# Kernel tuning notes

Hardware: AMD Instinct MI355X
Metric: run time of the kernel (lower is better)

Reference implementation:

```python
import jax, jax.numpy as jnp
import numpy as np
from functools import partial


def _normalise(v):
    return v / jnp.linalg.norm(v, axis=-1, keepdims=True)


def _orthogonalise(source, ref):
    # NOTE: faithful to original: divides by ||ref|| (not ||ref||^2)
    coef = jnp.einsum('bs,bs->b', source, ref) / jnp.linalg.norm(ref, axis=-1)
    return source - coef[:, None] * ref


def _skew(u):
    # (B,3) -> (B,3,3) cross-product matrix [u]_x, column j = u x e_j
    ux, uy, uz = u[:, 0], u[:, 1], u[:, 2]
    z = jnp.zeros_like(ux)
    return jnp.stack([
        jnp.stack([z, -uz, uy], axis=-1),
        jnp.stack([uz, z, -ux], axis=-1),
        jnp.stack([-uy, ux, z], axis=-1),
    ], axis=1)


def _rotate_frames(e0, e1, e2, angles, planar):
    u = e2 if planar else e1
    I = jnp.eye(3, dtype=u.dtype)[None]            # (1,3,3)
    cosA = jnp.cos(angles)[:, None, None]
    sinA = jnp.sin(angles)[:, None, None]
    outer = u[:, :, None] * u[:, None, :]          # (B,3,3)
    R = cosA * I + sinA * _skew(u) + (1.0 - cosA) * outer
    e0 = _normalise(jnp.einsum('bij,bj->bi', R, e0))
    if planar:
        e1 = _normalise(jnp.einsum('bij,bj->bi', R, e1))
    e1 = _normalise(_orthogonalise(e1, e0))
    e2 = _normalise(jnp.cross(e0, e1))
    return e0, e1, e2


def setup_inputs() -> dict:
    key = jax.random.key(0)
    B, N = 8192, 1024
    ks = jax.random.split(key, 6)
    x0 = jnp.zeros((B, 3), dtype=jnp.float32)
    e0 = _normalise(jax.random.uniform(ks[0], (B, 3), dtype=jnp.float32))
    e1 = _normalise(_orthogonalise(jax.random.uniform(ks[1], (B, 3), dtype=jnp.float32), e0))
    e2 = _normalise(jnp.cross(e0, e1))
    speeds = jax.random.uniform(ks[2], (B, N), dtype=jnp.float32)
    planar_angles = jax.random.normal(ks[3], (B, N), dtype=jnp.float32) * 0.3
    nonplanar_angles = jax.random.normal(ks[4], (B, N), dtype=jnp.float32) * 0.1
    return {'x0': x0, 'e0': e0, 'e1': e1, 'e2': e2,
            'speeds': speeds, 'planar_angles': planar_angles,
            'nonplanar_angles': nonplanar_angles, 'T': N, 'dt': 1}


def reference(x0, e0, e1, e2, speeds, planar_angles, nonplanar_angles, T, dt):
    n_steps = int(T / dt)
    B = x0.shape[0]
    ts = jnp.arange(n_steps, dtype=jnp.float32) * float(dt)

    def step(carry, inp):
        x, e0, e1, e2 = carry
        sp, pa, na = inp
        e0, e1, e2 = _rotate_frames(e0, e1, e2, pa, planar=True)
        e0, e1, e2 = _rotate_frames(e0, e1, e2, na, planar=False)
        x = x + sp[:, None] * e0
        return (x, e0, e1, e2), x

    xs = (speeds.T[:n_steps], planar_angles.T[:n_steps], nonplanar_angles.T[:n_steps])
    _, X = jax.lax.scan(step, (x0, e0, e1, e2), xs)
    X = jnp.transpose(X, (1, 0, 2))                 # (B, n_steps, 3)
    states = jnp.zeros((B, n_steps), dtype=jnp.float32)  # abstract state, left as zeros
    return ts, X, states, speeds, planar_angles, nonplanar_angles
```

## Files before the change

kernel.cpp:

```cpp
#include <hip/hip_runtime.h>

#define TPB   256
#define LSTEP 16


__global__ __launch_bounds__(TPB) void particle_scan_kernel(
    const float* __restrict__ x0p,
    const float* __restrict__ e0p,
    const float* __restrict__ e1p,
    const float* __restrict__ e2p,
    const float* __restrict__ sp,
    const float* __restrict__ pa,
    const float* __restrict__ na,
    const int*   __restrict__ dtp,
    float* __restrict__ out,
    int B, int N)
{
    const int tid  = threadIdx.x;
    const int lane = tid & 63;
    const int b    = (int)blockIdx.x * (TPB / 64) + (tid >> 6);
    const long long BN = (long long)B * N;
    const long long off_X      = N;
    const long long off_states = off_X + BN * 3;
    const long long off_speeds = off_states + BN;
    const long long off_pa     = off_speeds + BN;
    const long long off_na     = off_pa + BN;

    {
        int flat = (int)blockIdx.x * TPB + tid;
        if (flat < N) out[flat] = (float)flat * (float)dtp[0];
    }

    const long long base = (long long)b * N + (long long)lane * LSTEP;

    float spv[LSTEP], pav[LSTEP], nav[LSTEP];
    {
        const float4* s4 = reinterpret_cast<const float4*>(sp + base);
        const float4* p4 = reinterpret_cast<const float4*>(pa + base);
        const float4* q4 = reinterpret_cast<const float4*>(na + base);
        float4* os = reinterpret_cast<float4*>(out + off_speeds + base);
        float4* op = reinterpret_cast<float4*>(out + off_pa     + base);
        float4* oq = reinterpret_cast<float4*>(out + off_na     + base);
        float4* oz = reinterpret_cast<float4*>(out + off_states + base);
        const float4 z4 = make_float4(0.f, 0.f, 0.f, 0.f);
        #pragma unroll
        for (int i = 0; i < LSTEP / 4; ++i) {
            float4 a = s4[i], bb = p4[i], cc = q4[i];
            os[i] = a; op[i] = bb; oq[i] = cc; oz[i] = z4;
            spv[4*i+0] = a.x;  spv[4*i+1] = a.y;  spv[4*i+2] = a.z;  spv[4*i+3] = a.w;
            pav[4*i+0] = bb.x; pav[4*i+1] = bb.y; pav[4*i+2] = bb.z; pav[4*i+3] = bb.w;
            nav[4*i+0] = cc.x; nav[4*i+1] = cc.y; nav[4*i+2] = cc.z; nav[4*i+3] = cc.w;
        }
    }

    float a0x = 1.f, a0y = 0.f, a0z = 0.f;
    float a1x = 0.f, a1y = 1.f, a1z = 0.f;
    float a2x = 0.f, a2y = 0.f, a2z = 1.f;
    float dx = 0.f, dy = 0.f, dz = 0.f;
    #pragma unroll
    for (int t = 0; t < LSTEP; ++t) {
        float s1, c1, s2, c2;
        __sincosf(pav[t], &s1, &c1);
        __sincosf(nav[t], &s2, &c2);
        float t0x = c1*a0x + s1*a1x, t0y = c1*a0y + s1*a1y, t0z = c1*a0z + s1*a1z;
        float t1x = c1*a1x - s1*a0x, t1y = c1*a1y - s1*a0y, t1z = c1*a1z - s1*a0z;
        float u0x = c2*t0x - s2*a2x, u0y = c2*t0y - s2*a2y, u0z = c2*t0z - s2*a2z;
        float u2x = c2*a2x + s2*t0x, u2y = c2*a2y + s2*t0y, u2z = c2*a2z + s2*t0z;
        a0x = u0x; a0y = u0y; a0z = u0z;
        a1x = t1x; a1y = t1y; a1z = t1z;
        a2x = u2x; a2y = u2y; a2z = u2z;
        float s = spv[t];
        dx = fmaf(s, a0x, dx); dy = fmaf(s, a0y, dy); dz = fmaf(s, a0z, dz);
    }

    #define SCAN_STEP(K)                                                          \
    {                                                                             \
        float o0x=__shfl_up(a0x,K), o0y=__shfl_up(a0y,K), o0z=__shfl_up(a0z,K);   \
        float o1x=__shfl_up(a1x,K), o1y=__shfl_up(a1y,K), o1z=__shfl_up(a1z,K);   \
        float o2x=__shfl_up(a2x,K), o2y=__shfl_up(a2y,K), o2z=__shfl_up(a2z,K);   \
        float odx=__shfl_up(dx,K),  ody=__shfl_up(dy,K),  odz=__shfl_up(dz,K);    \
        if (lane >= K) {                                                          \
            float n0x = a0x*o0x + a0y*o1x + a0z*o2x;                              \
            float n0y = a0x*o0y + a0y*o1y + a0z*o2y;                              \
            float n0z = a0x*o0z + a0y*o1z + a0z*o2z;                              \
            float n1x = a1x*o0x + a1y*o1x + a1z*o2x;                              \
            float n1y = a1x*o0y + a1y*o1y + a1z*o2y;                              \
            float n1z = a1x*o0z + a1y*o1z + a1z*o2z;                              \
            float n2x = a2x*o0x + a2y*o1x + a2z*o2x;                              \
            float n2y = a2x*o0y + a2y*o1y + a2z*o2y;                              \
            float n2z = a2x*o0z + a2y*o1z + a2z*o2z;                              \
            float ndx = odx + dx*o0x + dy*o1x + dz*o2x;                           \
            float ndy = ody + dx*o0y + dy*o1y + dz*o2y;                           \
            float ndz = odz + dx*o0z + dy*o1z + dz*o2z;                           \
            a0x=n0x; a0y=n0y; a0z=n0z;                                            \
            a1x=n1x; a1y=n1y; a1z=n1z;                                            \
            a2x=n2x; a2y=n2y; a2z=n2z;                                            \
            dx=ndx; dy=ndy; dz=ndz;                                               \
        }                                                                         \
    }
    SCAN_STEP(1) SCAN_STEP(2) SCAN_STEP(4) SCAN_STEP(8) SCAN_STEP(16) SCAN_STEP(32)
    #undef SCAN_STEP

    {
        float e0x=__shfl_up(a0x,1), e0y=__shfl_up(a0y,1), e0z=__shfl_up(a0z,1);
        float e1x=__shfl_up(a1x,1), e1y=__shfl_up(a1y,1), e1z=__shfl_up(a1z,1);
        float e2x=__shfl_up(a2x,1), e2y=__shfl_up(a2y,1), e2z=__shfl_up(a2z,1);
        float edx=__shfl_up(dx,1),  edy=__shfl_up(dy,1),  edz=__shfl_up(dz,1);
        if (lane == 0) {
            e0x=1.f; e0y=0.f; e0z=0.f;
            e1x=0.f; e1y=1.f; e1z=0.f;
            e2x=0.f; e2y=0.f; e2z=1.f;
            edx=0.f; edy=0.f; edz=0.f;
        }
        a0x=e0x; a0y=e0y; a0z=e0z;
        a1x=e1x; a1y=e1y; a1z=e1z;
        a2x=e2x; a2y=e2y; a2z=e2z;
        dx=edx; dy=edy; dz=edz;
    }

    float f0x = e0p[3*b], f0y = e0p[3*b+1], f0z = e0p[3*b+2];
    float f1x = e1p[3*b], f1y = e1p[3*b+1], f1z = e1p[3*b+2];
    float f2x = e2p[3*b], f2y = e2p[3*b+1], f2z = e2p[3*b+2];
    float Xx  = x0p[3*b], Xy  = x0p[3*b+1], Xz  = x0p[3*b+2];

    float g0x = a0x*f0x + a0y*f1x + a0z*f2x;
    float g0y = a0x*f0y + a0y*f1y + a0z*f2y;
    float g0z = a0x*f0z + a0y*f1z + a0z*f2z;
    float g1x = a1x*f0x + a1y*f1x + a1z*f2x;
    float g1y = a1x*f0y + a1y*f1y + a1z*f2y;
    float g1z = a1x*f0z + a1y*f1z + a1z*f2z;
    float g2x = a2x*f0x + a2y*f1x + a2z*f2x;
    float g2y = a2x*f0y + a2y*f1y + a2z*f2y;
    float g2z = a2x*f0z + a2y*f1z + a2z*f2z;
    Xx += dx*f0x + dy*f1x + dz*f2x;
    Xy += dx*f0y + dy*f1y + dz*f2y;
    Xz += dx*f0z + dy*f1z + dz*f2z;

    float* Xb = out + off_X + base * 3;
    #pragma unroll
    for (int t = 0; t < LSTEP; ++t) {
        float s1, c1, s2, c2;
        __sincosf(pav[t], &s1, &c1);
        __sincosf(nav[t], &s2, &c2);
        float t0x = c1*g0x + s1*g1x, t0y = c1*g0y + s1*g1y, t0z = c1*g0z + s1*g1z;
        float t1x = c1*g1x - s1*g0x, t1y = c1*g1y - s1*g0y, t1z = c1*g1z - s1*g0z;
        float u0x = c2*t0x - s2*g2x, u0y = c2*t0y - s2*g2y, u0z = c2*t0z - s2*g2z;
        float u2x = c2*g2x + s2*t0x, u2y = c2*g2y + s2*t0y, u2z = c2*g2z + s2*t0z;
        g0x = u0x; g0y = u0y; g0z = u0z;
        g1x = t1x; g1y = t1y; g1z = t1z;
        g2x = u2x; g2y = u2y; g2z = u2z;
        float s = spv[t];
        Xx = fmaf(s, g0x, Xx); Xy = fmaf(s, g0y, Xy); Xz = fmaf(s, g0z, Xz);
        Xb[3*t + 0] = Xx;
        Xb[3*t + 1] = Xy;
        Xb[3*t + 2] = Xz;
    }
}

extern "C" void kernel_launch(void* const* d_in, const int* in_sizes, int n_in,
                              void* d_out, int out_size, void* d_ws, size_t ws_size,
                              hipStream_t stream)
{
    const float* x0  = (const float*)d_in[0];
    const float* e0i = (const float*)d_in[1];
    const float* e1i = (const float*)d_in[2];
    const float* e2i = (const float*)d_in[3];
    const float* sp  = (const float*)d_in[4];
    const float* pa  = (const float*)d_in[5];
    const float* na  = (const float*)d_in[6];
    const int*   dtp = (const int*)d_in[8];

    int B = in_sizes[0] / 3;
    int N = in_sizes[4] / B;

    int nBlocks = B / (TPB / 64);
    particle_scan_kernel<<<dim3(nBlocks), dim3(TPB), 0, stream>>>(
        x0, e0i, e1i, e2i, sp, pa, na, dtp, (float*)d_out, B, N);
}
```

Baseline: 371.3 us.

## Store local displacement prefixes and replay via frame transform with float4 stores

Measured after the change: 404.1 us. 1.09x slower.

```diff
diff --git a/kernel.cpp b/kernel.cpp
--- a/kernel.cpp
+++ b/kernel.cpp
@@ -33,7 +33,12 @@
 
     const long long base = (long long)b * N + (long long)lane * LSTEP;
 
-    float spv[LSTEP], pav[LSTEP], nav[LSTEP];
+    float a0x = 1.f, a0y = 0.f, a0z = 0.f;
+    float a1x = 0.f, a1y = 1.f, a1z = 0.f;
+    float a2x = 0.f, a2y = 0.f, a2z = 1.f;
+    float dx = 0.f, dy = 0.f, dz = 0.f;
+    float dlx[LSTEP], dly[LSTEP], dlz[LSTEP];
+
     {
         const float4* s4 = reinterpret_cast<const float4*>(sp + base);
         const float4* p4 = reinterpret_cast<const float4*>(pa + base);
@@ -43,34 +48,33 @@
         float4* oq = reinterpret_cast<float4*>(out + off_na     + base);
         float4* oz = reinterpret_cast<float4*>(out + off_states + base);
         const float4 z4 = make_float4(0.f, 0.f, 0.f, 0.f);
+
         #pragma unroll
-        for (int i = 0; i < LSTEP / 4; ++i) {
-            float4 a = s4[i], bb = p4[i], cc = q4[i];
-            os[i] = a; op[i] = bb; oq[i] = cc; oz[i] = z4;
-            spv[4*i+0] = a.x;  spv[4*i+1] = a.y;  spv[4*i+2] = a.z;  spv[4*i+3] = a.w;
-            pav[4*i+0] = bb.x; pav[4*i+1] = bb.y; pav[4*i+2] = bb.z; pav[4*i+3] = bb.w;
-            nav[4*i+0] = cc.x; nav[4*i+1] = cc.y; nav[4*i+2] = cc.z; nav[4*i+3] = cc.w;
+        for (int g = 0; g < LSTEP / 4; ++g) {
+            float4 sv = s4[g], pv = p4[g], qv = q4[g];
+            os[g] = sv; op[g] = pv; oq[g] = qv; oz[g] = z4;
+            float ss[4] = { sv.x, sv.y, sv.z, sv.w };
+            float pp[4] = { pv.x, pv.y, pv.z, pv.w };
+            float qq[4] = { qv.x, qv.y, qv.z, qv.w };
+            #pragma unroll
+            for (int j = 0; j < 4; ++j) {
+                const int t = 4 * g + j;
+                float s1, c1, s2, c2;
+                __sincosf(pp[j], &s1, &c1);
+                __sincosf(qq[j], &s2, &c2);
+                float t0x = c1*a0x + s1*a1x, t0y = c1*a0y + s1*a1y, t0z = c1*a0z + s1*a1z;
+                float t1x = c1*a1x - s1*a0x, t1y = c1*a1y - s1*a0y, t1z = c1*a1z - s1*a0z;
+                float u0x = c2*t0x - s2*a2x, u0y = c2*t0y - s2*a2y, u0z = c2*t0z - s2*a2z;
+                float u2x = c2*a2x + s2*t0x, u2y = c2*a2y + s2*t0y, u2z = c2*a2z + s2*t0z;
+                a0x = u0x; a0y = u0y; a0z = u0z;
+                a1x = t1x; a1y = t1y; a1z = t1z;
+                a2x = u2x; a2y = u2y; a2z = u2z;
+                dx = fmaf(ss[j], a0x, dx);
+                dy = fmaf(ss[j], a0y, dy);
+                dz = fmaf(ss[j], a0z, dz);
+                dlx[t] = dx; dly[t] = dy; dlz[t] = dz;
+            }
         }
-    }
-
-    float a0x = 1.f, a0y = 0.f, a0z = 0.f;
-    float a1x = 0.f, a1y = 1.f, a1z = 0.f;
-    float a2x = 0.f, a2y = 0.f, a2z = 1.f;
-    float dx = 0.f, dy = 0.f, dz = 0.f;
-    #pragma unroll
-    for (int t = 0; t < LSTEP; ++t) {
-        float s1, c1, s2, c2;
-        __sincosf(pav[t], &s1, &c1);
-        __sincosf(nav[t], &s2, &c2);
-        float t0x = c1*a0x + s1*a1x, t0y = c1*a0y + s1*a1y, t0z = c1*a0z + s1*a1z;
-        float t1x = c1*a1x - s1*a0x, t1y = c1*a1y - s1*a0y, t1z = c1*a1z - s1*a0z;
-        float u0x = c2*t0x - s2*a2x, u0y = c2*t0y - s2*a2y, u0z = c2*t0z - s2*a2z;
-        float u2x = c2*a2x + s2*t0x, u2y = c2*a2y + s2*t0y, u2z = c2*a2z + s2*t0z;
-        a0x = u0x; a0y = u0y; a0z = u0z;
-        a1x = t1x; a1y = t1y; a1z = t1z;
-        a2x = u2x; a2y = u2y; a2z = u2z;
-        float s = spv[t];
-        dx = fmaf(s, a0x, dx); dy = fmaf(s, a0y, dy); dz = fmaf(s, a0z, dz);
     }
 
     #define SCAN_STEP(K)                                                          \
@@ -138,22 +142,19 @@
 
     float* Xb = out + off_X + base * 3;
     #pragma unroll
-    for (int t = 0; t < LSTEP; ++t) {
-        float s1, c1, s2, c2;
-        __sincosf(pav[t], &s1, &c1);
-        __sincosf(nav[t], &s2, &c2);
-        float t0x = c1*g0x + s1*g1x, t0y = c1*g0y + s1*g1y, t0z = c1*g0z + s1*g1z;
-        float t1x = c1*g1x - s1*g0x, t1y = c1*g1y - s1*g0y, t1z = c1*g1z - s1*g0z;
-        float u0x = c2*t0x - s2*g2x, u0y = c2*t0y - s2*g2y, u0z = c2*t0z - s2*g2z;
-        float u2x = c2*g2x + s2*t0x, u2y = c2*g2y + s2*t0y, u2z = c2*g2z + s2*t0z;
-        g0x = u0x; g0y = u0y; g0z = u0z;
-        g1x = t1x; g1y = t1y; g1z = t1z;
-        g2x = u2x; g2y = u2y; g2z = u2z;
-        float s = spv[t];
-        Xx = fmaf(s, g0x, Xx); Xy = fmaf(s, g0y, Xy); Xz = fmaf(s, g0z, Xz);
-        Xb[3*t + 0] = Xx;
-        Xb[3*t + 1] = Xy;
-        Xb[3*t + 2] = Xz;
+    for (int g = 0; g < LSTEP / 4; ++g) {
+        float px[12];
+        #pragma unroll
+        for (int j = 0; j < 4; ++j) {
+            const int t = 4 * g + j;
+            px[3*j+0] = fmaf(dlx[t], g0x, fmaf(dly[t], g1x, fmaf(dlz[t], g2x, Xx)));
+            px[3*j+1] = fmaf(dlx[t], g0y, fmaf(dly[t], g1y, fmaf(dlz[t], g2y, Xy)));
+            px[3*j+2] = fmaf(dlx[t], g0z, fmaf(dly[t], g1z, fmaf(dlz[t], g2z, Xz)));
+        }
+        float4* o4 = reinterpret_cast<float4*>(Xb + 12 * g);
+        o4[0] = make_float4(px[0], px[1],  px[2],  px[3]);
+        o4[1] = make_float4(px[4], px[5],  px[6],  px[7]);
+        o4[2] = make_float4(px[8], px[9],  px[10], px[11]);
     }
 }
 
```
